# Kernel tuning notes

Hardware: AMD Instinct MI355X
Metric: run time of the kernel (lower is better)

The kernel has to match this reference:

```python
import jax, jax.numpy as jnp
import numpy as np

SIGMA = 1.0


def _rbf_kernel(X, sigma):
    # pairwise squared Euclidean distances: ||xi||^2 + ||xj||^2 - 2 xi.xj
    sq = jnp.sum(X * X, axis=1)  # [n]
    d2 = sq[:, None] + sq[None, :] - 2.0 * (X @ X.T)
    d2 = jnp.maximum(d2, 0.0)
    return jnp.exp(-d2 / (2.0 * sigma ** 2))


def _center(K):
    # Kc = H @ K @ H with H = I - 11^T/n, done in O(n^2):
    # Kc = K - row_mean - col_mean + grand_mean
    row_mean = jnp.mean(K, axis=1, keepdims=True)   # [n,1]
    col_mean = jnp.mean(K, axis=0, keepdims=True)   # [1,n]
    grand = jnp.mean(K)
    return K - row_mean - col_mean + grand


def setup_inputs() -> dict:
    key = jax.random.key(0)
    k1, k2 = jax.random.split(key)
    X = jax.random.normal(k1, (8192, 512), dtype=jnp.float32)
    Y = jax.random.normal(k2, (8192, 512), dtype=jnp.float32)
    return {"X": X, "Y": Y}


def reference(X, Y):
    n = X.shape[0]
    K = _rbf_kernel(X, SIGMA)
    L = _rbf_kernel(Y, SIGMA)
    Kc = _center(K)
    Lc = _center(L)
    # trace(Kc @ Lc) == sum(Kc * Lc^T) == sum(Kc * Lc) since Lc symmetric
    hsic_value = jnp.sum(Kc * Lc) / (n - 1) ** 2
    return hsic_value
```

## Files before the change

### kernel.cpp

```cpp
#include <hip/hip_runtime.h>
#include <hip/hip_bf16.h>

#define N 8192
#define D 512
#define NKT 8

typedef __attribute__((ext_vector_type(4))) float f32x4;
typedef __attribute__((ext_vector_type(2))) long i64x2;

__device__ __forceinline__ void g2l16(const void* g, void* l) {
  __builtin_amdgcn_global_load_lds(
      (const __attribute__((address_space(1))) void*)g,
      (__attribute__((address_space(3))) void*)l, 16, 0, 0);
}

__global__ __launch_bounds__(128) void prep_kernel(
    const float* __restrict__ X, const float* __restrict__ Y,
    unsigned char* __restrict__ Xb, unsigned char* __restrict__ Yb,
    float* __restrict__ sqX, float* __restrict__ sqY) {
  const int b = blockIdx.x;
  const int row = b & (N - 1);
  const float* src = (b < N) ? X : Y;
  unsigned char* dst = (b < N) ? Xb : Yb;
  float* sq = (b < N) ? sqX : sqY;
  const int t = threadIdx.x;
  float4 v = reinterpret_cast<const float4*>(src + (size_t)row * D)[t];
  unsigned p = __builtin_amdgcn_cvt_pk_fp8_f32(v.x, v.y, 0, false);
  p = __builtin_amdgcn_cvt_pk_fp8_f32(v.z, v.w, p, true);
  float f0 = __builtin_amdgcn_cvt_f32_fp8(p, 0);
  float f1 = __builtin_amdgcn_cvt_f32_fp8(p, 1);
  float f2 = __builtin_amdgcn_cvt_f32_fp8(p, 2);
  float f3 = __builtin_amdgcn_cvt_f32_fp8(p, 3);
  float s = f0 * f0 + f1 * f1 + f2 * f2 + f3 * f3;
  const int g = t >> 4;
  const int kl = (t & 15) * 4;
  const int dest = g * 64 + ((kl & 31) >> 3) * 16 + (kl >> 5) * 8 + (kl & 7);
  *reinterpret_cast<unsigned*>(dst + (size_t)row * D + dest) = p;
  #pragma unroll
  for (int msk = 1; msk < 64; msk <<= 1) s += __shfl_xor(s, msk);
  __shared__ float red[2];
  if ((t & 63) == 0) red[t >> 6] = s;
  __syncthreads();
  if (t == 0) sq[row] = red[0] + red[1];
}

__global__ __launch_bounds__(256, 2) void hsic_main(
    const unsigned char* __restrict__ Xb, const unsigned char* __restrict__ Yb,
    const float* __restrict__ sqX, const float* __restrict__ sqY,
    float* __restrict__ rowK, float* __restrict__ rowL,
    float* __restrict__ sums) {
  __shared__ __align__(16) unsigned char sXi[128 * 64];
  __shared__ __align__(16) unsigned char sXj[128 * 64];
  __shared__ __align__(16) unsigned char sYi[128 * 64];
  __shared__ __align__(16) unsigned char sYj[128 * 64];

  const int bid = (blockIdx.x & 7) * 260 + (blockIdx.x >> 3);
  int ti = (int)((129.0f - sqrtf(16641.0f - 8.0f * (float)bid)) * 0.5f);
  while (ti > 0 && (ti * (129 - ti)) / 2 > bid) --ti;
  while (((ti + 1) * (128 - ti)) / 2 <= bid) ++ti;
  const int tj = ti + (bid - (ti * (129 - ti)) / 2);
  const bool diag = (ti == tj);

  const int ib = ti * 128, jb = tj * 128;
  const int t = threadIdx.x;
  const int lane = t & 63, wave = t >> 6;
  const int wr = wave >> 1, wc = wave & 1;
  const int fr = lane & 15, fq = lane >> 4;

  f32x4 accK[4][4], accL[4][4];
  #pragma unroll
  for (int m = 0; m < 4; ++m)
    #pragma unroll
    for (int n = 0; n < 4; ++n) { accK[m][n] = (f32x4)0.f; accL[m][n] = (f32x4)0.f; }

  const unsigned char* s0 = Xb + (size_t)ib * D;
  const unsigned char* s1 = Xb + (size_t)jb * D;
  const unsigned char* s2 = Yb + (size_t)ib * D;
  const unsigned char* s3 = Yb + (size_t)jb * D;

  const int srow = t >> 2;
  const int swcb = ((t & 3) * 16) ^ (((t >> 3) & 3) << 4);
  const int lo16 = t * 16;

  auto stageX = [&](int kt) {
    #pragma unroll
    for (int q = 0; q < 2; ++q) {
      const size_t goff = (size_t)(q * 64 + srow) * D + kt * 64 + swcb;
      const int lo = q * 4096 + lo16;
      g2l16(s0 + goff, sXi + lo);
      g2l16(s1 + goff, sXj + lo);
    }
  };
  auto stageY = [&](int kt) {
    #pragma unroll
    for (int q = 0; q < 2; ++q) {
      const size_t goff = (size_t)(q * 64 + srow) * D + kt * 64 + swcb;
      const int lo = q * 4096 + lo16;
      g2l16(s2 + goff, sYi + lo);
      g2l16(s3 + goff, sYj + lo);
    }
  };

  const int fcol = (fq * 16) ^ (((fr >> 1) & 3) << 4);

  i64x2 a[4], b[4];
  auto loadFrags = [&](const unsigned char* si, const unsigned char* sj) {
    #pragma unroll
    for (int m = 0; m < 4; ++m)
      a[m] = *(const i64x2*)&si[(wr * 64 + m * 16 + fr) * 64 + fcol];
    #pragma unroll
    for (int n = 0; n < 4; ++n)
      b[n] = *(const i64x2*)&sj[(wc * 64 + n * 16 + fr) * 64 + fcol];
  };
  auto mmaInto = [&](f32x4 (&acc)[4][4]) {
    __builtin_amdgcn_s_setprio(1);
    #pragma unroll
    for (int m = 0; m < 4; ++m)
      #pragma unroll
      for (int n = 0; n < 4; ++n) {
        acc[m][n] = __builtin_amdgcn_mfma_f32_16x16x32_fp8_fp8(a[m][0], b[n][0], acc[m][n], 0, 0, 0);
        acc[m][n] = __builtin_amdgcn_mfma_f32_16x16x32_fp8_fp8(a[m][1], b[n][1], acc[m][n], 0, 0, 0);
      }
    __builtin_amdgcn_s_setprio(0);
  };

  stageX(0);
  stageY(0);
  for (int kt = 0; kt < NKT - 1; ++kt) {
    asm volatile("s_waitcnt vmcnt(4)" ::: "memory");
    __builtin_amdgcn_s_barrier();
    loadFrags(sXi, sXj);
    asm volatile("s_waitcnt lgkmcnt(0)" ::: "memory");
    __builtin_amdgcn_s_barrier();
    stageX(kt + 1);
    mmaInto(accK);
    asm volatile("s_waitcnt vmcnt(4)" ::: "memory");
    __builtin_amdgcn_s_barrier();
    loadFrags(sYi, sYj);
    asm volatile("s_waitcnt lgkmcnt(0)" ::: "memory");
    __builtin_amdgcn_s_barrier();
    stageY(kt + 1);
    mmaInto(accL);
  }
  asm volatile("s_waitcnt vmcnt(4)" ::: "memory");
  __builtin_amdgcn_s_barrier();
  loadFrags(sXi, sXj);
  mmaInto(accK);
  asm volatile("s_waitcnt vmcnt(0)" ::: "memory");
  __builtin_amdgcn_s_barrier();
  loadFrags(sYi, sYj);
  mmaInto(accL);

  float sxj[4], syj[4];
  #pragma unroll
  for (int n = 0; n < 4; ++n) {
    const int j = jb + wc * 64 + n * 16 + fr;
    sxj[n] = sqX[j];
    syj[n] = sqY[j];
  }
  float kl = 0.f;
  float ckK[4] = {0.f, 0.f, 0.f, 0.f}, ckL[4] = {0.f, 0.f, 0.f, 0.f};
  #pragma unroll
  for (int m = 0; m < 4; ++m) {
    #pragma unroll
    for (int r = 0; r < 4; ++r) {
      const int i = ib + wr * 64 + m * 16 + fq * 4 + r;
      const float sxi = sqX[i], syi = sqY[i];
      float rk = 0.f, rl = 0.f;
      #pragma unroll
      for (int n = 0; n < 4; ++n) {
        float dK = fmaxf(sxi + sxj[n] - 2.f * accK[m][n][r], 0.f);
        float Kv = __expf(-0.5f * dK);
        float dL = fmaxf(syi + syj[n] - 2.f * accL[m][n][r], 0.f);
        float Lv = __expf(-0.5f * dL);
        kl += Kv * Lv;
        rk += Kv; rl += Lv;
        ckK[n] += Kv; ckL[n] += Lv;
      }
      #pragma unroll
      for (int msk = 1; msk < 16; msk <<= 1) {
        rk += __shfl_xor(rk, msk);
        rl += __shfl_xor(rl, msk);
      }
      if (fr == 0) {
        atomicAdd(&rowK[i], rk);
        atomicAdd(&rowL[i], rl);
      }
    }
  }
  if (!diag) {
    #pragma unroll
    for (int n = 0; n < 4; ++n) {
      float a2 = ckK[n], b2 = ckL[n];
      a2 += __shfl_xor(a2, 16); a2 += __shfl_xor(a2, 32);
      b2 += __shfl_xor(b2, 16); b2 += __shfl_xor(b2, 32);
      if (fq == 0) {
        const int j = jb + wc * 64 + n * 16 + fr;
        atomicAdd(&rowK[j], a2);
        atomicAdd(&rowL[j], b2);
      }
    }
    kl *= 2.f;
  }
  #pragma unroll
  for (int msk = 1; msk < 64; msk <<= 1) kl += __shfl_xor(kl, msk);
  __shared__ float klred[4];
  if (lane == 0) klred[wave] = kl;
  __syncthreads();
  if (t == 0) atomicAdd(sums, klred[0] + klred[1] + klred[2] + klred[3]);
}

__global__ __launch_bounds__(256) void finalize_kernel(
    const float* __restrict__ rowK, const float* __restrict__ rowL,
    const float* __restrict__ sums, float* __restrict__ out) {
  const int t = threadIdx.x;
  float dp = 0.f, sk = 0.f, sl = 0.f;
  for (int i = t; i < N; i += 256) {
    float a = rowK[i], b = rowL[i];
    dp += a * b; sk += a; sl += b;
  }
  #pragma unroll
  for (int msk = 1; msk < 64; msk <<= 1) {
    dp += __shfl_xor(dp, msk);
    sk += __shfl_xor(sk, msk);
    sl += __shfl_xor(sl, msk);
  }
  __shared__ float r[3][4];
  const int wave = t >> 6, lane = t & 63;
  if (lane == 0) { r[0][wave] = dp; r[1][wave] = sk; r[2][wave] = sl; }
  __syncthreads();
  if (t == 0) {
    float DP = r[0][0] + r[0][1] + r[0][2] + r[0][3];
    float SK = r[1][0] + r[1][1] + r[1][2] + r[1][3];
    float SL = r[2][0] + r[2][1] + r[2][2] + r[2][3];
    const float n = (float)N;
    float raw = sums[0] - (2.f / n) * DP + (SK / n) * (SL / n);
    out[0] = raw / ((n - 1.f) * (n - 1.f));
  }
}

extern "C" void kernel_launch(void* const* d_in, const int* in_sizes, int n_in,
                              void* d_out, int out_size, void* d_ws, size_t ws_size,
                              hipStream_t stream) {
  const float* X = (const float*)d_in[0];
  const float* Y = (const float*)d_in[1];
  char* ws = (char*)d_ws;
  unsigned char* Xb = (unsigned char*)ws;
  unsigned char* Yb = (unsigned char*)(ws + (size_t)N * D);
  float* sqX = (float*)(ws + (size_t)2 * N * D);
  float* sqY = sqX + N;
  float* rowK = sqY + N;
  float* rowL = rowK + N;
  float* sums = rowL + N;

  hipMemsetAsync(rowK, 0, (size_t)(2 * N + 16) * sizeof(float), stream);
  prep_kernel<<<2 * N, 128, 0, stream>>>(X, Y, Xb, Yb, sqX, sqY);
  const int ntiles = (N / 128) * (N / 128 + 1) / 2;
  hsic_main<<<ntiles, 256, 0, stream>>>(Xb, Yb, sqX, sqY, rowK, rowL, sums);
  finalize_kernel<<<1, 256, 0, stream>>>(rowK, rowL, sums, (float*)d_out);
}
```

Baseline: 154.0 us.

## Double K-tile depth to 128 and restructure staging into X/Y ping-pong buffers

After: 150.6 us. 1.02x faster.

```diff
diff --git a/kernel.cpp b/kernel.cpp
--- a/kernel.cpp
+++ b/kernel.cpp
@@ -3,10 +3,12 @@
 
 #define N 8192
 #define D 512
-#define NKT 8
 
 typedef __attribute__((ext_vector_type(4))) float f32x4;
 typedef __attribute__((ext_vector_type(2))) long i64x2;
+
+#define WAITVM(n) asm volatile("s_waitcnt vmcnt(" #n ")" ::: "memory")
+#define BAR __builtin_amdgcn_s_barrier()
 
 __device__ __forceinline__ void g2l16(const void* g, void* l) {
   __builtin_amdgcn_global_load_lds(
@@ -49,10 +51,7 @@
     const float* __restrict__ sqX, const float* __restrict__ sqY,
     float* __restrict__ rowK, float* __restrict__ rowL,
     float* __restrict__ sums) {
-  __shared__ __align__(16) unsigned char sXi[128 * 64];
-  __shared__ __align__(16) unsigned char sXj[128 * 64];
-  __shared__ __align__(16) unsigned char sYi[128 * 64];
-  __shared__ __align__(16) unsigned char sYj[128 * 64];
+  __shared__ __align__(16) unsigned char sbuf[2][2][128 * 128];
 
   const int bid = (blockIdx.x & 7) * 260 + (blockIdx.x >> 3);
   int ti = (int)((129.0f - sqrtf(16641.0f - 8.0f * (float)bid)) * 0.5f);
@@ -78,78 +77,73 @@
   const unsigned char* s2 = Yb + (size_t)ib * D;
   const unsigned char* s3 = Yb + (size_t)jb * D;
 
-  const int srow = t >> 2;
-  const int swcb = ((t & 3) * 16) ^ (((t >> 3) & 3) << 4);
+  const int srow = t >> 3;
+  const int swcb = ((t & 7) * 16) ^ (((t >> 3) & 7) << 4);
   const int lo16 = t * 16;
 
-  auto stageX = [&](int kt) {
-    #pragma unroll
-    for (int q = 0; q < 2; ++q) {
-      const size_t goff = (size_t)(q * 64 + srow) * D + kt * 64 + swcb;
+  auto stage = [&](int ph) {
+    const int kt = ph >> 1;
+    const unsigned char* si = (ph & 1) ? s2 : s0;
+    const unsigned char* sj = (ph & 1) ? s3 : s1;
+    unsigned char* di = sbuf[ph & 1][0];
+    unsigned char* dj = sbuf[ph & 1][1];
+    #pragma unroll
+    for (int q = 0; q < 4; ++q) {
+      const size_t goff = (size_t)(q * 32 + srow) * D + kt * 128 + swcb;
       const int lo = q * 4096 + lo16;
-      g2l16(s0 + goff, sXi + lo);
-      g2l16(s1 + goff, sXj + lo);
+      g2l16(si + goff, di + lo);
+      g2l16(sj + goff, dj + lo);
     }
   };
-  auto stageY = [&](int kt) {
-    #pragma unroll
-    for (int q = 0; q < 2; ++q) {
-      const size_t goff = (size_t)(q * 64 + srow) * D + kt * 64 + swcb;
-      const int lo = q * 4096 + lo16;
-      g2l16(s2 + goff, sYi + lo);
-      g2l16(s3 + goff, sYj + lo);
+
+  auto compute = [&](const unsigned char* si, const unsigned char* sj,
+                     f32x4 (&acc)[4][4]) {
+    #pragma unroll
+    for (int kk = 0; kk < 2; ++kk) {
+      const int csel = kk * 64 + fq * 16;
+      i64x2 a[4], b[4];
+      #pragma unroll
+      for (int m = 0; m < 4; ++m) {
+        const int row = wr * 64 + m * 16 + fr;
+        a[m] = *(const i64x2*)&si[row * 128 + (csel ^ ((fr & 7) << 4))];
+      }
+      #pragma unroll
+      for (int n = 0; n < 4; ++n) {
+        const int row = wc * 64 + n * 16 + fr;
+        b[n] = *(const i64x2*)&sj[row * 128 + (csel ^ ((fr & 7) << 4))];
+      }
+      __builtin_amdgcn_s_setprio(1);
+      #pragma unroll
+      for (int m = 0; m < 4; ++m)
+        #pragma unroll
+        for (int n = 0; n < 4; ++n) {
+          acc[m][n] = __builtin_amdgcn_mfma_f32_16x16x32_fp8_fp8(a[m][0], b[n][0], acc[m][n], 0, 0, 0);
+          acc[m][n] = __builtin_amdgcn_mfma_f32_16x16x32_fp8_fp8(a[m][1], b[n][1], acc[m][n], 0, 0, 0);
+        }
+      __builtin_amdgcn_s_setprio(0);
     }
   };
 
-  const int fcol = (fq * 16) ^ (((fr >> 1) & 3) << 4);
-
-  i64x2 a[4], b[4];
-  auto loadFrags = [&](const unsigned char* si, const unsigned char* sj) {
-    #pragma unroll
-    for (int m = 0; m < 4; ++m)
-      a[m] = *(const i64x2*)&si[(wr * 64 + m * 16 + fr) * 64 + fcol];
-    #pragma unroll
-    for (int n = 0; n < 4; ++n)
-      b[n] = *(const i64x2*)&sj[(wc * 64 + n * 16 + fr) * 64 + fcol];
-  };
-  auto mmaInto = [&](f32x4 (&acc)[4][4]) {
-    __builtin_amdgcn_s_setprio(1);
-    #pragma unroll
-    for (int m = 0; m < 4; ++m)
-      #pragma unroll
-      for (int n = 0; n < 4; ++n) {
-        acc[m][n] = __builtin_amdgcn_mfma_f32_16x16x32_fp8_fp8(a[m][0], b[n][0], acc[m][n], 0, 0, 0);
-        acc[m][n] = __builtin_amdgcn_mfma_f32_16x16x32_fp8_fp8(a[m][1], b[n][1], acc[m][n], 0, 0, 0);
-      }
-    __builtin_amdgcn_s_setprio(0);
-  };
-
-  stageX(0);
-  stageY(0);
-  for (int kt = 0; kt < NKT - 1; ++kt) {
-    asm volatile("s_waitcnt vmcnt(4)" ::: "memory");
-    __builtin_amdgcn_s_barrier();
-    loadFrags(sXi, sXj);
-    asm volatile("s_waitcnt lgkmcnt(0)" ::: "memory");
-    __builtin_amdgcn_s_barrier();
-    stageX(kt + 1);
-    mmaInto(accK);
-    asm volatile("s_waitcnt vmcnt(4)" ::: "memory");
-    __builtin_amdgcn_s_barrier();
-    loadFrags(sYi, sYj);
-    asm volatile("s_waitcnt lgkmcnt(0)" ::: "memory");
-    __builtin_amdgcn_s_barrier();
-    stageY(kt + 1);
-    mmaInto(accL);
-  }
-  asm volatile("s_waitcnt vmcnt(4)" ::: "memory");
-  __builtin_amdgcn_s_barrier();
-  loadFrags(sXi, sXj);
-  mmaInto(accK);
-  asm volatile("s_waitcnt vmcnt(0)" ::: "memory");
-  __builtin_amdgcn_s_barrier();
-  loadFrags(sYi, sYj);
-  mmaInto(accL);
+  stage(0); stage(1);
+  #pragma unroll 1
+  for (int kt = 0; kt < 3; ++kt) {
+    WAITVM(8);
+    BAR;
+    compute(sbuf[0][0], sbuf[0][1], accK);
+    BAR;
+    stage(2 * kt + 2);
+    WAITVM(8);
+    BAR;
+    compute(sbuf[1][0], sbuf[1][1], accL);
+    BAR;
+    stage(2 * kt + 3);
+  }
+  WAITVM(8);
+  BAR;
+  compute(sbuf[0][0], sbuf[0][1], accK);
+  WAITVM(0);
+  BAR;
+  compute(sbuf[1][0], sbuf[1][1], accL);
 
   float sxj[4], syj[4];
   #pragma unroll
```
